# Kernel optimization log

Hardware: AMD Instinct MI355X
Metric: run time of the kernel (lower is better)

## Reference

```python
import jax, jax.numpy as jnp
import numpy as np

B, T, I, H = 64, 512, 1024, 1024


def setup_inputs() -> dict:
    key = jax.random.key(0)
    ks = jax.random.split(key, 6)
    s_ih = 1.0 / np.sqrt(I)
    s_hh = 1.0 / np.sqrt(H)
    x = jax.random.normal(ks[0], (B, T, I), dtype=jnp.float32)
    w_ih = jax.random.uniform(ks[1], (4 * H, I), minval=-s_ih, maxval=s_ih, dtype=jnp.float32)
    b_ih = jax.random.uniform(ks[2], (4 * H,), minval=-s_ih, maxval=s_ih, dtype=jnp.float32)
    w_hh = jax.random.uniform(ks[3], (4 * H, H), minval=-s_hh, maxval=s_hh, dtype=jnp.float32)
    b_hh = jax.random.uniform(ks[4], (4 * H,), minval=-s_hh, maxval=s_hh, dtype=jnp.float32)
    # forget_bias = logit(u), u ~ Uniform(1/H, 1-1/H), as in init_hidden
    u = jax.random.uniform(ks[5], (H,), minval=1.0 / H, maxval=1.0 - 1.0 / H, dtype=jnp.float32)
    forget_bias = jnp.log(u / (1.0 - u))
    h0 = jnp.zeros((B, H), dtype=jnp.float32)
    c0 = jnp.zeros((B, H), dtype=jnp.float32)
    return {"x": x, "w_ih": w_ih, "b_ih": b_ih, "w_hh": w_hh, "b_hh": b_hh,
            "forget_bias": forget_bias, "h0": h0, "c0": c0}


def reference(x, w_ih, b_ih, w_hh, b_hh, forget_bias, h0, c0):
    Hd = forget_bias.shape[0]
    # Precompute input projection for all timesteps: [T, B, 4H]
    xW = jnp.einsum('bti,gi->tbg', x, w_ih) + b_ih

    def step(carry, xw_t):
        h, c = carry
        lin = xw_t + h @ w_hh.T + b_hh  # [B, 4H]
        r, f, u, o = jnp.split(lin, 4, axis=1)
        r = jax.nn.sigmoid(r - forget_bias)
        f = jax.nn.sigmoid(f + forget_bias)
        u = jnp.tanh(u)
        o = jax.nn.sigmoid(o)
        g = r * (1.0 - (1.0 - f) ** 2) + (1.0 - r) * f ** 2  # UR gate
        c = g * c + (1.0 - g) * u
        h = o * jnp.tanh(c)
        return (h, c), h

    (h_t, c_t), out = jax.lax.scan(step, (h0, c0), xW)
    out = jnp.swapaxes(out, 0, 1)  # [B, T, H]
    return out, h_t[None], c_t[None]  # h/c with num_layers=1 leading dim
```

## Files before the change

kernel.cpp:

```cpp
#include <hip/hip_runtime.h>
#include <stdint.h>
#include <stddef.h>

typedef __attribute__((ext_vector_type(8))) short short8;
typedef __attribute__((ext_vector_type(4))) float f32x4;
typedef __attribute__((ext_vector_type(2))) float f32x2;

#define MFMA16(A, B, C) __builtin_amdgcn_mfma_f32_16x16x32_bf16((A), (B), (C), 0, 0, 0)

static const size_t OFF_XB   = 0;
static const size_t OFF_WIH  = 67108864;
static const size_t OFF_WHH  = 75497472;
static const size_t OFF_BIAS = 83886080;
static const size_t OFF_H0   = 83902464;
static const size_t OFF_H1   = 84033536;
static const size_t OFF_FLG  = 84164608;
static const size_t OFF_XW   = 84426752;
static const size_t XW_F32_BYTES = 536870912;

__device__ __forceinline__ unsigned short f2bf(float f) {
    union { float f; uint32_t u; } v; v.f = f;
    uint32_t u = v.u;
    u += 0x7FFFu + ((u >> 16) & 1u);
    return (unsigned short)(u >> 16);
}
__device__ __forceinline__ float bf2f(unsigned short b) {
    union { uint32_t u; float f; } v; v.u = ((uint32_t)b) << 16;
    return v.f;
}

__device__ __forceinline__ float fast_sigmoid(float x) {
    return 1.f / (1.f + __expf(-x));
}
__device__ __forceinline__ float fast_tanh(float x) {
    return 1.f - 2.f / (__expf(2.f * x) + 1.f);
}

__global__ __launch_bounds__(256) void cast4_kernel(const float* __restrict__ s,
                                                    unsigned short* __restrict__ d, int n4) {
    int i = blockIdx.x * 256 + threadIdx.x;
    if (i >= n4) return;
    float4 f = ((const float4*)s)[i];
    ushort4 o;
    o.x = f2bf(f.x); o.y = f2bf(f.y); o.z = f2bf(f.z); o.w = f2bf(f.w);
    ((ushort4*)d)[i] = o;
}

__global__ __launch_bounds__(256) void init_misc(const float* __restrict__ b_ih,
                                                 const float* __restrict__ b_hh,
                                                 float* __restrict__ bias,
                                                 const float* __restrict__ h0,
                                                 unsigned short* __restrict__ h_ini,
                                                 unsigned int* __restrict__ flags) {
    int i = blockIdx.x * 256 + threadIdx.x;
    if (i < 512) flags[i] = 0u;
    if (i < 4096) bias[i] = b_ih[i] + b_hh[i];
    if (i < 65536) h_ini[i] = f2bf(h0[i]);
}

template <bool XWF32>
__global__ __launch_bounds__(256) void xw_gemm(const unsigned short* __restrict__ xb,
                                               const unsigned short* __restrict__ wb,
                                               const float* __restrict__ bias,
                                               void* __restrict__ xw) {
    __shared__ __align__(16) unsigned short As[128 * 32];
    __shared__ __align__(16) unsigned short Bs[128 * 32];
    const int bm = blockIdx.x, bn = blockIdx.y;
    const int tid = threadIdx.x;
    const int wave = tid >> 6, lane = tid & 63;
    const int wm = (wave >> 1) * 64, wn = (wave & 1) * 64;
    const int lr = lane & 15, lk = (lane >> 4) * 8;

    const int c0 = tid, c1 = tid + 256;
    const int r0 = c0 >> 2, k0c = (c0 & 3) * 8;
    const int r1 = c1 >> 2, k1c = (c1 & 3) * 8;
    const int mA0 = bm * 128 + r0, mA1 = bm * 128 + r1;
    const unsigned short* pa0 = xb + (size_t)(((mA0 & 63) << 9) + (mA0 >> 6)) * 1024 + k0c;
    const unsigned short* pa1 = xb + (size_t)(((mA1 & 63) << 9) + (mA1 >> 6)) * 1024 + k1c;
    const unsigned short* pb0 = wb + (size_t)(bn * 128 + r0) * 1024 + k0c;
    const unsigned short* pb1 = wb + (size_t)(bn * 128 + r1) * 1024 + k1c;
    unsigned short* sa0 = As + r0 * 32 + k0c;
    unsigned short* sa1 = As + r1 * 32 + k1c;
    unsigned short* sb0 = Bs + r0 * 32 + k0c;
    unsigned short* sb1 = Bs + r1 * 32 + k1c;

    f32x4 acc[4][4] = {};

    for (int kk = 0; kk < 32; ++kk) {
        const int ko = kk * 32;
        uint4 av0 = *(const uint4*)(pa0 + ko);
        uint4 av1 = *(const uint4*)(pa1 + ko);
        uint4 bv0 = *(const uint4*)(pb0 + ko);
        uint4 bv1 = *(const uint4*)(pb1 + ko);
        __syncthreads();
        *(uint4*)sa0 = av0;
        *(uint4*)sa1 = av1;
        *(uint4*)sb0 = bv0;
        *(uint4*)sb1 = bv1;
        __syncthreads();
        short8 af[4], bfr[4];
#pragma unroll
        for (int mi = 0; mi < 4; ++mi)
            af[mi] = *(const short8*)(As + (wm + mi * 16 + lr) * 32 + lk);
#pragma unroll
        for (int ni = 0; ni < 4; ++ni)
            bfr[ni] = *(const short8*)(Bs + (wn + ni * 16 + lr) * 32 + lk);
#pragma unroll
        for (int mi = 0; mi < 4; ++mi)
#pragma unroll
            for (int ni = 0; ni < 4; ++ni)
                acc[mi][ni] = MFMA16(af[mi], bfr[ni], acc[mi][ni]);
    }

    const int rbase = (lane >> 4) * 4;
#pragma unroll
    for (int ni = 0; ni < 4; ++ni) {
        const int gc = bn * 128 + wn + ni * 16 + lr;
        const float bv = bias[gc];
#pragma unroll
        for (int mi = 0; mi < 4; ++mi) {
            const int gr = bm * 128 + wm + mi * 16 + rbase;
#pragma unroll
            for (int r = 0; r < 4; ++r) {
                float v = acc[mi][ni][r] + bv;
                if (XWF32) ((float*)xw)[(size_t)(gr + r) * 4096 + gc] = v;
                else ((unsigned short*)xw)[(size_t)(gr + r) * 4096 + gc] = f2bf(v);
            }
        }
    }
}

template <bool XWF32>
__global__ __launch_bounds__(512, 2) void lstm_persistent(
        unsigned short* hb0, unsigned short* hb1,
        const void* __restrict__ xw,
        const unsigned short* __restrict__ whh,
        const float* __restrict__ fb,
        const float* __restrict__ c0,
        float* __restrict__ out,
        float* __restrict__ hcout,
        unsigned int* ctr) {
    __shared__ __align__(16) float part[8 * 64 * 64];

    const int tid = threadIdx.x;
    const int wave = tid >> 6, lane = tid & 63;
    const int bk = blockIdx.x, ch0 = bk * 16;
    const int kq = wave;
    const int lr = lane & 15, g = lane >> 4;

    short8 Wf[4][4];
#pragma unroll
    for (int ni = 0; ni < 4; ++ni)
#pragma unroll
        for (int ks = 0; ks < 4; ++ks) {
            const unsigned short* p = whh + (size_t)(ni * 1024 + ch0 + lr) * 1024
                                          + kq * 128 + ks * 32 + g * 8;
            asm volatile("global_load_dwordx4 %0, %1, off"
                         : "=&v"(Wf[ni][ks]) : "v"(p));
        }
    asm volatile("s_waitcnt vmcnt(0)" ::: "memory");
    __builtin_amdgcn_sched_barrier(0);

    const int b  = tid >> 3;
    const int j0 = 2 * (tid & 7);
    const int ch = ch0 + j0;
    const float fb0 = fb[ch], fb1 = fb[ch + 1];
    float c0r = c0[b * 1024 + ch], c1r = c0[b * 1024 + ch + 1];

    int wsl[4];
#pragma unroll
    for (int oi = 0; oi < 4; ++oi)
        wsl[oi] = kq * 4096 + lr * 64 + (((oi * 4 + g) ^ (lr & 7)) * 4);
    int rsl[4];
#pragma unroll
    for (int g4 = 0; g4 < 4; ++g4)
        rsl[g4] = b * 64 + (((g4 * 4 + (j0 >> 2)) ^ (b & 7)) * 4) + (j0 & 3);

    const float* xwf = (const float*)xw + (size_t)b * 4096 + ch;
    const unsigned short* xwb = (const unsigned short*)xw + (size_t)b * 4096 + ch;
    float* orun = out + (size_t)b * 524288 + ch;
    unsigned int* my_sig  = &ctr[(bk >> 3) * 32];
    unsigned int* my_poll = &ctr[kq * 32];

    float xwv0[4], xwv1[4];
#pragma unroll
    for (int g4 = 0; g4 < 4; ++g4) {
        if constexpr (XWF32) {
            const f32x2 v = *(const f32x2*)(xwf + g4 * 1024);
            xwv0[g4] = v.x; xwv1[g4] = v.y;
        } else {
            const uint32_t u = *(const uint32_t*)(xwb + g4 * 1024);
            xwv0[g4] = bf2f((unsigned short)u);
            xwv1[g4] = bf2f((unsigned short)(u >> 16));
        }
    }

    float h0v = 0.f, h1v = 0.f;

    for (int t = 0; t < 512; ++t) {
        const unsigned short* hp = (t & 1) ? hb1 : hb0;
        unsigned short* hn       = (t & 1) ? hb0 : hb1;

        if (t > 0) {
            const unsigned tgt = (unsigned)t * 8u;
            while (__hip_atomic_load(my_poll, __ATOMIC_RELAXED,
                                     __HIP_MEMORY_SCOPE_AGENT) < tgt) {}
        }
        __builtin_amdgcn_sched_barrier(0);

        short8 af[4][4];
        {
            const unsigned short* hbase = hp + (size_t)lr * 1024 + kq * 128 + g * 8;
#pragma unroll
            for (int bi = 0; bi < 4; ++bi) {
                const unsigned short* p = hbase + (size_t)bi * 16 * 1024;
                asm volatile(
                    "global_load_dwordx4 %0, %4, off sc1\n\t"
                    "global_load_dwordx4 %1, %4, off offset:64 sc1\n\t"
                    "global_load_dwordx4 %2, %4, off offset:128 sc1\n\t"
                    "global_load_dwordx4 %3, %4, off offset:192 sc1"
                    : "=&v"(af[bi][0]), "=&v"(af[bi][1]),
                      "=&v"(af[bi][2]), "=&v"(af[bi][3])
                    : "v"(p));
            }
        }
        asm volatile("s_waitcnt vmcnt(0)" ::: "memory");
        __builtin_amdgcn_sched_barrier(0);

        f32x4 acc[4][4] = {};
#pragma unroll
        for (int ks = 0; ks < 4; ++ks)
#pragma unroll
            for (int oi = 0; oi < 4; ++oi)
#pragma unroll
                for (int bi = 0; bi < 4; ++bi)
                    acc[oi][bi] = MFMA16(Wf[oi][ks], af[bi][ks], acc[oi][bi]);

#pragma unroll
        for (int oi = 0; oi < 4; ++oi)
#pragma unroll
            for (int bi = 0; bi < 4; ++bi)
                *(f32x4*)&part[wsl[oi] + bi * 1024] = acc[oi][bi];
        __syncthreads();

        float l0[4], l1[4];
#pragma unroll
        for (int g4 = 0; g4 < 4; ++g4) {
            float s0 = xwv0[g4], s1 = xwv1[g4];
#pragma unroll
            for (int k8 = 0; k8 < 8; ++k8) {
                const float2 v = *(const float2*)&part[k8 * 4096 + rsl[g4]];
                s0 += v.x; s1 += v.y;
            }
            l0[g4] = s0; l1[g4] = s1;
        }
        const float rg0 = fast_sigmoid(l0[0] - fb0);
        const float fg0 = fast_sigmoid(l0[1] + fb0);
        const float ug0 = fast_tanh(l0[2]);
        const float og0 = fast_sigmoid(l0[3]);
        const float rg1 = fast_sigmoid(l1[0] - fb1);
        const float fg1 = fast_sigmoid(l1[1] + fb1);
        const float ug1 = fast_tanh(l1[2]);
        const float og1 = fast_sigmoid(l1[3]);
        const float of0 = 1.f - fg0, of1 = 1.f - fg1;
        const float gg0 = rg0 * (1.f - of0 * of0) + (1.f - rg0) * (fg0 * fg0);
        const float gg1 = rg1 * (1.f - of1 * of1) + (1.f - rg1) * (fg1 * fg1);
        c0r = gg0 * c0r + (1.f - gg0) * ug0;
        c1r = gg1 * c1r + (1.f - gg1) * ug1;
        h0v = og0 * fast_tanh(c0r);
        h1v = og1 * fast_tanh(c1r);

        const unsigned hw = ((unsigned)f2bf(h1v) << 16) | (unsigned)f2bf(h0v);
        __hip_atomic_store((unsigned int*)&hn[b * 1024 + ch], hw,
                           __ATOMIC_RELAXED, __HIP_MEMORY_SCOPE_AGENT);

        __syncthreads();
        if (tid == 0)
            __hip_atomic_fetch_add(my_sig, 1u, __ATOMIC_RELAXED,
                                   __HIP_MEMORY_SCOPE_AGENT);
        __builtin_amdgcn_sched_barrier(0);

        *(f32x2*)orun = (f32x2){h0v, h1v};
        orun += 1024;
        {
            const int tp = (t < 511) ? t + 1 : 511;
#pragma unroll
            for (int g4 = 0; g4 < 4; ++g4) {
                if constexpr (XWF32) {
                    const f32x2 v = *(const f32x2*)(xwf + (size_t)tp * 262144 + g4 * 1024);
                    xwv0[g4] = v.x; xwv1[g4] = v.y;
                } else {
                    const uint32_t u = *(const uint32_t*)(xwb + (size_t)tp * 262144 + g4 * 1024);
                    xwv0[g4] = bf2f((unsigned short)u);
                    xwv1[g4] = bf2f((unsigned short)(u >> 16));
                }
            }
        }
        asm volatile("s_waitcnt vmcnt(0)" ::: "memory");
        __builtin_amdgcn_sched_barrier(0);
    }

    *(f32x2*)&hcout[b * 1024 + ch] = (f32x2){h0v, h1v};
    *(f32x2*)&hcout[65536 + b * 1024 + ch] = (f32x2){c0r, c1r};
}

extern "C" void kernel_launch(void* const* d_in, const int* in_sizes, int n_in,
                              void* d_out, int out_size, void* d_ws, size_t ws_size,
                              hipStream_t stream) {
    const float* x   = (const float*)d_in[0];
    const float* wih = (const float*)d_in[1];
    const float* bih = (const float*)d_in[2];
    const float* whh = (const float*)d_in[3];
    const float* bhh = (const float*)d_in[4];
    const float* fb  = (const float*)d_in[5];
    const float* h0  = (const float*)d_in[6];
    const float* c0  = (const float*)d_in[7];

    char* ws = (char*)d_ws;
    float* out = (float*)d_out;
    float* hc  = out + 33554432;

    unsigned short* xb   = (unsigned short*)(ws + OFF_XB);
    unsigned short* wihb = (unsigned short*)(ws + OFF_WIH);
    unsigned short* whhb = (unsigned short*)(ws + OFF_WHH);
    float* bias          = (float*)(ws + OFF_BIAS);
    unsigned short* hb0  = (unsigned short*)(ws + OFF_H0);
    unsigned short* hb1  = (unsigned short*)(ws + OFF_H1);
    unsigned int* flags  = (unsigned int*)(ws + OFF_FLG);
    void* xw             = (void*)(ws + OFF_XW);

    const bool f32path = ws_size >= OFF_XW + XW_F32_BYTES;

    cast4_kernel<<<32768, 256, 0, stream>>>(x, xb, 8388608);
    cast4_kernel<<<4096, 256, 0, stream>>>(wih, wihb, 1048576);
    cast4_kernel<<<4096, 256, 0, stream>>>(whh, whhb, 1048576);
    init_misc<<<256, 256, 0, stream>>>(bih, bhh, bias, h0, hb0, flags);

    dim3 g(256, 32);
    if (f32path) xw_gemm<true><<<g, 256, 0, stream>>>(xb, wihb, bias, xw);
    else         xw_gemm<false><<<g, 256, 0, stream>>>(xb, wihb, bias, xw);

    const float* fbp = fb;
    const float* c0p = c0;
    void* xwp = xw;
    const unsigned short* whhp = whhb;
    unsigned int* ctr = flags;
    void* kargs[] = { &hb0, &hb1, &xwp, &whhp, &fbp, &c0p, &out, &hc, &ctr };
    if (f32path)
        hipLaunchCooperativeKernel((void*)lstm_persistent<true>, dim3(64), dim3(512),
                                   kargs, 0, stream);
    else
        hipLaunchCooperativeKernel((void*)lstm_persistent<false>, dim3(64), dim3(512),
                                   kargs, 0, stream);
}
```

Measured before the change: 4.169 ms.

## Split batch into two halves with separate flags to overlap recurrent phases

Each timestep is now processed as two 32-row batch halves, each with its own arrival counter. The B-half loads are issued before the A-half's reduction and gate math, and the A-half's h is published with its own signal before the B-half MFMAs run. The aim is to let other blocks start the next step on half A while half B is still computing, hiding inter-block sync latency. The cost is twice as many barriers, polls and atomics per step, narrower scalar stores, and reliance on the counter array being large enough for a second bank at offset 256.

```diff
diff --git a/kernel.cpp b/kernel.cpp
--- a/kernel.cpp
+++ b/kernel.cpp
@@ -140,7 +140,7 @@
         float* __restrict__ out,
         float* __restrict__ hcout,
         unsigned int* ctr) {
-    __shared__ __align__(16) float part[8 * 64 * 64];
+    __shared__ __align__(16) float part[8 * 32 * 64];
 
     const int tid = threadIdx.x;
     const int wave = tid >> 6, lane = tid & 63;
@@ -161,147 +161,209 @@
     asm volatile("s_waitcnt vmcnt(0)" ::: "memory");
     __builtin_amdgcn_sched_barrier(0);
 
-    const int b  = tid >> 3;
-    const int j0 = 2 * (tid & 7);
-    const int ch = ch0 + j0;
-    const float fb0 = fb[ch], fb1 = fb[ch + 1];
-    float c0r = c0[b * 1024 + ch], c1r = c0[b * 1024 + ch + 1];
+    const int jj = tid & 15;
+    const int bb = tid >> 4;
+    const int ch = ch0 + jj;
+    const float fbv = fb[ch];
+    float cA = c0[bb * 1024 + ch];
+    float cB = c0[(32 + bb) * 1024 + ch];
 
     int wsl[4];
 #pragma unroll
     for (int oi = 0; oi < 4; ++oi)
-        wsl[oi] = kq * 4096 + lr * 64 + (((oi * 4 + g) ^ (lr & 7)) * 4);
+        wsl[oi] = kq * 2048 + lr * 64 + ((((oi * 4 + g) ^ (lr & 7))) << 2);
     int rsl[4];
 #pragma unroll
     for (int g4 = 0; g4 < 4; ++g4)
-        rsl[g4] = b * 64 + (((g4 * 4 + (j0 >> 2)) ^ (b & 7)) * 4) + (j0 & 3);
-
-    const float* xwf = (const float*)xw + (size_t)b * 4096 + ch;
-    const unsigned short* xwb = (const unsigned short*)xw + (size_t)b * 4096 + ch;
-    float* orun = out + (size_t)b * 524288 + ch;
-    unsigned int* my_sig  = &ctr[(bk >> 3) * 32];
-    unsigned int* my_poll = &ctr[kq * 32];
-
-    float xwv0[4], xwv1[4];
+        rsl[g4] = bb * 64 + ((((g4 * 4 + (jj >> 2)) ^ (bb & 7))) << 2) + (jj & 3);
+
+    const float* xw32 = (const float*)xw;
+    const unsigned short* xw16 = (const unsigned short*)xw;
+    const size_t xbA = (size_t)bb * 4096 + ch;
+    const size_t xbB = (size_t)(32 + bb) * 4096 + ch;
+    float* orA = out + (size_t)bb * 524288 + ch;
+    float* orB = out + (size_t)(32 + bb) * 524288 + ch;
+    unsigned int* sigA = &ctr[(bk >> 3) * 32];
+    unsigned int* sigB = &ctr[256 + (bk >> 3) * 32];
+    unsigned int* polA = &ctr[kq * 32];
+    unsigned int* polB = &ctr[256 + kq * 32];
+
+    float xwA[4], xwB[4];
 #pragma unroll
     for (int g4 = 0; g4 < 4; ++g4) {
         if constexpr (XWF32) {
-            const f32x2 v = *(const f32x2*)(xwf + g4 * 1024);
-            xwv0[g4] = v.x; xwv1[g4] = v.y;
+            xwA[g4] = xw32[xbA + g4 * 1024];
+            xwB[g4] = xw32[xbB + g4 * 1024];
         } else {
-            const uint32_t u = *(const uint32_t*)(xwb + g4 * 1024);
-            xwv0[g4] = bf2f((unsigned short)u);
-            xwv1[g4] = bf2f((unsigned short)(u >> 16));
+            xwA[g4] = bf2f(xw16[xbA + g4 * 1024]);
+            xwB[g4] = bf2f(xw16[xbB + g4 * 1024]);
         }
     }
 
-    float h0v = 0.f, h1v = 0.f;
+    float hA = 0.f, hB = 0.f;
 
     for (int t = 0; t < 512; ++t) {
         const unsigned short* hp = (t & 1) ? hb1 : hb0;
         unsigned short* hn       = (t & 1) ? hb0 : hb1;
+        const unsigned short* hbase = hp + (size_t)lr * 1024 + kq * 128 + g * 8;
 
         if (t > 0) {
             const unsigned tgt = (unsigned)t * 8u;
-            while (__hip_atomic_load(my_poll, __ATOMIC_RELAXED,
+            while (__hip_atomic_load(polA, __ATOMIC_RELAXED,
                                      __HIP_MEMORY_SCOPE_AGENT) < tgt) {}
         }
         __builtin_amdgcn_sched_barrier(0);
 
-        short8 af[4][4];
+        short8 afA[2][4];
+#pragma unroll
+        for (int bi = 0; bi < 2; ++bi) {
+            const unsigned short* p = hbase + (size_t)bi * 16 * 1024;
+            asm volatile(
+                "global_load_dwordx4 %0, %4, off sc1\n\t"
+                "global_load_dwordx4 %1, %4, off offset:64 sc1\n\t"
+                "global_load_dwordx4 %2, %4, off offset:128 sc1\n\t"
+                "global_load_dwordx4 %3, %4, off offset:192 sc1"
+                : "=&v"(afA[bi][0]), "=&v"(afA[bi][1]),
+                  "=&v"(afA[bi][2]), "=&v"(afA[bi][3])
+                : "v"(p));
+        }
+        asm volatile("s_waitcnt vmcnt(0)" ::: "memory");
+        __builtin_amdgcn_sched_barrier(0);
+
         {
-            const unsigned short* hbase = hp + (size_t)lr * 1024 + kq * 128 + g * 8;
-#pragma unroll
-            for (int bi = 0; bi < 4; ++bi) {
-                const unsigned short* p = hbase + (size_t)bi * 16 * 1024;
-                asm volatile(
-                    "global_load_dwordx4 %0, %4, off sc1\n\t"
-                    "global_load_dwordx4 %1, %4, off offset:64 sc1\n\t"
-                    "global_load_dwordx4 %2, %4, off offset:128 sc1\n\t"
-                    "global_load_dwordx4 %3, %4, off offset:192 sc1"
-                    : "=&v"(af[bi][0]), "=&v"(af[bi][1]),
-                      "=&v"(af[bi][2]), "=&v"(af[bi][3])
-                    : "v"(p));
+            f32x4 acc[4][2] = {};
+#pragma unroll
+            for (int ks = 0; ks < 4; ++ks)
+#pragma unroll
+                for (int oi = 0; oi < 4; ++oi)
+#pragma unroll
+                    for (int bi = 0; bi < 2; ++bi)
+                        acc[oi][bi] = MFMA16(Wf[oi][ks], afA[bi][ks], acc[oi][bi]);
+#pragma unroll
+            for (int oi = 0; oi < 4; ++oi)
+#pragma unroll
+                for (int bi = 0; bi < 2; ++bi)
+                    *(f32x4*)&part[wsl[oi] + bi * 1024] = acc[oi][bi];
+        }
+        __syncthreads();
+
+        if (t > 0) {
+            const unsigned tgt = (unsigned)t * 8u;
+            while (__hip_atomic_load(polB, __ATOMIC_RELAXED,
+                                     __HIP_MEMORY_SCOPE_AGENT) < tgt) {}
+        }
+        __builtin_amdgcn_sched_barrier(0);
+        short8 afB[2][4];
+#pragma unroll
+        for (int bi = 0; bi < 2; ++bi) {
+            const unsigned short* p = hbase + (size_t)(32 + bi * 16) * 1024;
+            asm volatile(
+                "global_load_dwordx4 %0, %4, off sc1\n\t"
+                "global_load_dwordx4 %1, %4, off offset:64 sc1\n\t"
+                "global_load_dwordx4 %2, %4, off offset:128 sc1\n\t"
+                "global_load_dwordx4 %3, %4, off offset:192 sc1"
+                : "=&v"(afB[bi][0]), "=&v"(afB[bi][1]),
+                  "=&v"(afB[bi][2]), "=&v"(afB[bi][3])
+                : "v"(p));
+        }
+        __builtin_amdgcn_sched_barrier(0);
+
+        {
+            float l[4];
+#pragma unroll
+            for (int g4 = 0; g4 < 4; ++g4) {
+                float s = xwA[g4];
+#pragma unroll
+                for (int k8 = 0; k8 < 8; ++k8)
+                    s += part[k8 * 2048 + rsl[g4]];
+                l[g4] = s;
             }
+            const float rg = fast_sigmoid(l[0] - fbv);
+            const float fg = fast_sigmoid(l[1] + fbv);
+            const float ug = fast_tanh(l[2]);
+            const float og = fast_sigmoid(l[3]);
+            const float of = 1.f - fg;
+            const float gg = rg * (1.f - of * of) + (1.f - rg) * (fg * fg);
+            cA = gg * cA + (1.f - gg) * ug;
+            hA = og * fast_tanh(cA);
+            const unsigned hw = (unsigned)f2bf(hA);
+            asm volatile("global_store_short %0, %1, off sc1"
+                         :: "v"(hn + bb * 1024 + ch), "v"(hw) : "memory");
         }
         asm volatile("s_waitcnt vmcnt(0)" ::: "memory");
-        __builtin_amdgcn_sched_barrier(0);
-
-        f32x4 acc[4][4] = {};
-#pragma unroll
-        for (int ks = 0; ks < 4; ++ks)
+        __syncthreads();
+        if (tid == 0)
+            __hip_atomic_fetch_add(sigA, 1u, __ATOMIC_RELAXED, __HIP_MEMORY_SCOPE_AGENT);
+        __builtin_amdgcn_sched_barrier(0);
+
+        {
+            f32x4 acc[4][2] = {};
+#pragma unroll
+            for (int ks = 0; ks < 4; ++ks)
+#pragma unroll
+                for (int oi = 0; oi < 4; ++oi)
+#pragma unroll
+                    for (int bi = 0; bi < 2; ++bi)
+                        acc[oi][bi] = MFMA16(Wf[oi][ks], afB[bi][ks], acc[oi][bi]);
 #pragma unroll
             for (int oi = 0; oi < 4; ++oi)
 #pragma unroll
-                for (int bi = 0; bi < 4; ++bi)
-                    acc[oi][bi] = MFMA16(Wf[oi][ks], af[bi][ks], acc[oi][bi]);
-
-#pragma unroll
-        for (int oi = 0; oi < 4; ++oi)
-#pragma unroll
-            for (int bi = 0; bi < 4; ++bi)
-                *(f32x4*)&part[wsl[oi] + bi * 1024] = acc[oi][bi];
-        __syncthreads();
-
-        float l0[4], l1[4];
-#pragma unroll
-        for (int g4 = 0; g4 < 4; ++g4) {
-            float s0 = xwv0[g4], s1 = xwv1[g4];
-#pragma unroll
-            for (int k8 = 0; k8 < 8; ++k8) {
-                const float2 v = *(const float2*)&part[k8 * 4096 + rsl[g4]];
-                s0 += v.x; s1 += v.y;
+                for (int bi = 0; bi < 2; ++bi)
+                    *(f32x4*)&part[wsl[oi] + bi * 1024] = acc[oi][bi];
+        }
+        __syncthreads();
+
+        {
+            float l[4];
+#pragma unroll
+            for (int g4 = 0; g4 < 4; ++g4) {
+                float s = xwB[g4];
+#pragma unroll
+                for (int k8 = 0; k8 < 8; ++k8)
+                    s += part[k8 * 2048 + rsl[g4]];
+                l[g4] = s;
             }
-            l0[g4] = s0; l1[g4] = s1;
-        }
-        const float rg0 = fast_sigmoid(l0[0] - fb0);
-        const float fg0 = fast_sigmoid(l0[1] + fb0);
-        const float ug0 = fast_tanh(l0[2]);
-        const float og0 = fast_sigmoid(l0[3]);
-        const float rg1 = fast_sigmoid(l1[0] - fb1);
-        const float fg1 = fast_sigmoid(l1[1] + fb1);
-        const float ug1 = fast_tanh(l1[2]);
-        const float og1 = fast_sigmoid(l1[3]);
-        const float of0 = 1.f - fg0, of1 = 1.f - fg1;
-        const float gg0 = rg0 * (1.f - of0 * of0) + (1.f - rg0) * (fg0 * fg0);
-        const float gg1 = rg1 * (1.f - of1 * of1) + (1.f - rg1) * (fg1 * fg1);
-        c0r = gg0 * c0r + (1.f - gg0) * ug0;
-        c1r = gg1 * c1r + (1.f - gg1) * ug1;
-        h0v = og0 * fast_tanh(c0r);
-        h1v = og1 * fast_tanh(c1r);
-
-        const unsigned hw = ((unsigned)f2bf(h1v) << 16) | (unsigned)f2bf(h0v);
-        __hip_atomic_store((unsigned int*)&hn[b * 1024 + ch], hw,
-                           __ATOMIC_RELAXED, __HIP_MEMORY_SCOPE_AGENT);
-
+            const float rg = fast_sigmoid(l[0] - fbv);
+            const float fg = fast_sigmoid(l[1] + fbv);
+            const float ug = fast_tanh(l[2]);
+            const float og = fast_sigmoid(l[3]);
+            const float of = 1.f - fg;
+            const float gg = rg * (1.f - of * of) + (1.f - rg) * (fg * fg);
+            cB = gg * cB + (1.f - gg) * ug;
+            hB = og * fast_tanh(cB);
+            const unsigned hw = (unsigned)f2bf(hB);
+            asm volatile("global_store_short %0, %1, off sc1"
+                         :: "v"(hn + (32 + bb) * 1024 + ch), "v"(hw) : "memory");
+        }
+        asm volatile("s_waitcnt vmcnt(0)" ::: "memory");
         __syncthreads();
         if (tid == 0)
-            __hip_atomic_fetch_add(my_sig, 1u, __ATOMIC_RELAXED,
-                                   __HIP_MEMORY_SCOPE_AGENT);
-        __builtin_amdgcn_sched_barrier(0);
-
-        *(f32x2*)orun = (f32x2){h0v, h1v};
-        orun += 1024;
+            __hip_atomic_fetch_add(sigB, 1u, __ATOMIC_RELAXED, __HIP_MEMORY_SCOPE_AGENT);
+        __builtin_amdgcn_sched_barrier(0);
+
+        *orA = hA; orA += 1024;
+        *orB = hB; orB += 1024;
         {
             const int tp = (t < 511) ? t + 1 : 511;
+            const size_t tb = (size_t)tp * 262144;
 #pragma unroll
             for (int g4 = 0; g4 < 4; ++g4) {
                 if constexpr (XWF32) {
-                    const f32x2 v = *(const f32x2*)(xwf + (size_t)tp * 262144 + g4 * 1024);
-                    xwv0[g4] = v.x; xwv1[g4] = v.y;
+                    xwA[g4] = xw32[tb + xbA + g4 * 1024];
+                    xwB[g4] = xw32[tb + xbB + g4 * 1024];
                 } else {
-                    const uint32_t u = *(const uint32_t*)(xwb + (size_t)tp * 262144 + g4 * 1024);
-                    xwv0[g4] = bf2f((unsigned short)u);
-                    xwv1[g4] = bf2f((unsigned short)(u >> 16));
+                    xwA[g4] = bf2f(xw16[tb + xbA + g4 * 1024]);
+                    xwB[g4] = bf2f(xw16[tb + xbB + g4 * 1024]);
                 }
             }
         }
-        asm volatile("s_waitcnt vmcnt(0)" ::: "memory");
         __builtin_amdgcn_sched_barrier(0);
     }
 
-    *(f32x2*)&hcout[b * 1024 + ch] = (f32x2){h0v, h1v};
-    *(f32x2*)&hcout[65536 + b * 1024 + ch] = (f32x2){c0r, c1r};
+    hcout[bb * 1024 + ch] = hA;
+    hcout[65536 + bb * 1024 + ch] = cA;
+    hcout[(32 + bb) * 1024 + ch] = hB;
+    hcout[65536 + (32 + bb) * 1024 + ch] = cB;
 }
 
 extern "C" void kernel_launch(void* const* d_in, const int* in_sizes, int n_in,
```

Result: slower. 4.626 ms (+11.0%).

## Fuse input-projection GEMM into persistent LSTM kernel with producer/consumer flags

Applied to the files above, without the earlier changes.

Merges the xW GEMM into the cooperative recurrence kernel: 64 blocks run the LSTM recurrence while 192 extra blocks compute xW tiles in time order and signal per-row-block progress counters that the recurrent blocks poll before loading each timestep. The x fp32-to-bf16 cast is folded into the GEMM tile load, which removes the separate cast pass and the extra bf16 copy of x. The goal is to overlap the large projection GEMM with the serial recurrence. In exchange, the GEMM blocks compete with the recurrent blocks for memory bandwidth and CUs. The recurrence may also stall on progress flags if the GEMM falls behind. The flag region now shares the init flag array at offset 256.

```diff
diff --git a/kernel.cpp b/kernel.cpp
--- a/kernel.cpp
+++ b/kernel.cpp
@@ -8,7 +8,6 @@
 
 #define MFMA16(A, B, C) __builtin_amdgcn_mfma_f32_16x16x32_bf16((A), (B), (C), 0, 0, 0)
 
-static const size_t OFF_XB   = 0;
 static const size_t OFF_WIH  = 67108864;
 static const size_t OFF_WHH  = 75497472;
 static const size_t OFF_BIAS = 83886080;
@@ -59,94 +58,103 @@
 }
 
 template <bool XWF32>
-__global__ __launch_bounds__(256) void xw_gemm(const unsigned short* __restrict__ xb,
-                                               const unsigned short* __restrict__ wb,
-                                               const float* __restrict__ bias,
-                                               void* __restrict__ xw) {
-    __shared__ __align__(16) unsigned short As[128 * 32];
-    __shared__ __align__(16) unsigned short Bs[128 * 32];
-    const int bm = blockIdx.x, bn = blockIdx.y;
-    const int tid = threadIdx.x;
-    const int wave = tid >> 6, lane = tid & 63;
-    const int wm = (wave >> 1) * 64, wn = (wave & 1) * 64;
-    const int lr = lane & 15, lk = (lane >> 4) * 8;
-
-    const int c0 = tid, c1 = tid + 256;
-    const int r0 = c0 >> 2, k0c = (c0 & 3) * 8;
-    const int r1 = c1 >> 2, k1c = (c1 & 3) * 8;
-    const int mA0 = bm * 128 + r0, mA1 = bm * 128 + r1;
-    const unsigned short* pa0 = xb + (size_t)(((mA0 & 63) << 9) + (mA0 >> 6)) * 1024 + k0c;
-    const unsigned short* pa1 = xb + (size_t)(((mA1 & 63) << 9) + (mA1 >> 6)) * 1024 + k1c;
-    const unsigned short* pb0 = wb + (size_t)(bn * 128 + r0) * 1024 + k0c;
-    const unsigned short* pb1 = wb + (size_t)(bn * 128 + r1) * 1024 + k1c;
-    unsigned short* sa0 = As + r0 * 32 + k0c;
-    unsigned short* sa1 = As + r1 * 32 + k1c;
-    unsigned short* sb0 = Bs + r0 * 32 + k0c;
-    unsigned short* sb1 = Bs + r1 * 32 + k1c;
-
-    f32x4 acc[4][4] = {};
-
-    for (int kk = 0; kk < 32; ++kk) {
-        const int ko = kk * 32;
-        uint4 av0 = *(const uint4*)(pa0 + ko);
-        uint4 av1 = *(const uint4*)(pa1 + ko);
-        uint4 bv0 = *(const uint4*)(pb0 + ko);
-        uint4 bv1 = *(const uint4*)(pb1 + ko);
-        __syncthreads();
-        *(uint4*)sa0 = av0;
-        *(uint4*)sa1 = av1;
-        *(uint4*)sb0 = bv0;
-        *(uint4*)sb1 = bv1;
-        __syncthreads();
-        short8 af[4], bfr[4];
-#pragma unroll
-        for (int mi = 0; mi < 4; ++mi)
-            af[mi] = *(const short8*)(As + (wm + mi * 16 + lr) * 32 + lk);
-#pragma unroll
-        for (int ni = 0; ni < 4; ++ni)
-            bfr[ni] = *(const short8*)(Bs + (wn + ni * 16 + lr) * 32 + lk);
-#pragma unroll
-        for (int mi = 0; mi < 4; ++mi)
-#pragma unroll
-            for (int ni = 0; ni < 4; ++ni)
-                acc[mi][ni] = MFMA16(af[mi], bfr[ni], acc[mi][ni]);
-    }
-
-    const int rbase = (lane >> 4) * 4;
-#pragma unroll
-    for (int ni = 0; ni < 4; ++ni) {
-        const int gc = bn * 128 + wn + ni * 16 + lr;
-        const float bv = bias[gc];
-#pragma unroll
-        for (int mi = 0; mi < 4; ++mi) {
-            const int gr = bm * 128 + wm + mi * 16 + rbase;
-#pragma unroll
-            for (int r = 0; r < 4; ++r) {
-                float v = acc[mi][ni][r] + bv;
-                if (XWF32) ((float*)xw)[(size_t)(gr + r) * 4096 + gc] = v;
-                else ((unsigned short*)xw)[(size_t)(gr + r) * 4096 + gc] = f2bf(v);
-            }
-        }
-    }
-}
-
-template <bool XWF32>
-__global__ __launch_bounds__(512, 2) void lstm_persistent(
+__global__ __launch_bounds__(512, 2) void fused_kernel(
         unsigned short* hb0, unsigned short* hb1,
-        const void* __restrict__ xw,
+        void* xw,
         const unsigned short* __restrict__ whh,
+        const unsigned short* __restrict__ wih,
+        const float* __restrict__ x,
+        const float* __restrict__ bias,
         const float* __restrict__ fb,
         const float* __restrict__ c0,
         float* __restrict__ out,
         float* __restrict__ hcout,
-        unsigned int* ctr) {
-    __shared__ __align__(16) float part[8 * 64 * 64];
-
+        unsigned int* flags) {
+    __shared__ __align__(16) char smem[131072];
     const int tid = threadIdx.x;
     const int wave = tid >> 6, lane = tid & 63;
+    unsigned int* xwprog = flags + 256;
+
+    if (blockIdx.x >= 64) {
+        unsigned short* As = (unsigned short*)smem;
+        unsigned short* Bs = (unsigned short*)(smem + 8192);
+        const int g = blockIdx.x - 64;
+        const int wm = (wave & 3) * 32, wn = (wave >> 2) * 64;
+        const int lr = lane & 15, lk = (lane >> 4) * 8;
+        const int r0 = tid >> 2, k0c = (tid & 3) * 8;
+        const int rbase = (lane >> 4) * 4;
+
+        for (int tau = g; tau < 8192; tau += 192) {
+            const int bm = tau >> 5, bn = tau & 31;
+            const int m = bm * 128 + r0;
+            const float* pax = x + (size_t)((m & 63) * 512 + (m >> 6)) * 1024 + k0c;
+            const unsigned short* pbw = wih + (size_t)(bn * 128 + r0) * 1024 + k0c;
+            unsigned short* sa = As + r0 * 32 + k0c;
+            unsigned short* sb = Bs + r0 * 32 + k0c;
+
+            f32x4 acc[2][4] = {};
+            for (int kk = 0; kk < 32; ++kk) {
+                const int ko = kk * 32;
+                float4 a0 = *(const float4*)(pax + ko);
+                float4 a1 = *(const float4*)(pax + ko + 4);
+                uint4 bv = *(const uint4*)(pbw + ko);
+                __syncthreads();
+                ushort4 ca, cb;
+                ca.x = f2bf(a0.x); ca.y = f2bf(a0.y); ca.z = f2bf(a0.z); ca.w = f2bf(a0.w);
+                cb.x = f2bf(a1.x); cb.y = f2bf(a1.y); cb.z = f2bf(a1.z); cb.w = f2bf(a1.w);
+                *(ushort4*)sa = ca;
+                *(ushort4*)(sa + 4) = cb;
+                *(uint4*)sb = bv;
+                __syncthreads();
+                short8 af0 = *(const short8*)(As + (wm + lr) * 32 + lk);
+                short8 af1 = *(const short8*)(As + (wm + 16 + lr) * 32 + lk);
+                short8 bf4[4];
+#pragma unroll
+                for (int ni = 0; ni < 4; ++ni)
+                    bf4[ni] = *(const short8*)(Bs + (wn + ni * 16 + lr) * 32 + lk);
+#pragma unroll
+                for (int ni = 0; ni < 4; ++ni) {
+                    acc[0][ni] = MFMA16(af0, bf4[ni], acc[0][ni]);
+                    acc[1][ni] = MFMA16(af1, bf4[ni], acc[1][ni]);
+                }
+            }
+#pragma unroll
+            for (int ni = 0; ni < 4; ++ni) {
+                const int gc = bn * 128 + wn + ni * 16 + lr;
+                const float bvs = bias[gc];
+#pragma unroll
+                for (int mi = 0; mi < 2; ++mi) {
+                    const int gr = bm * 128 + wm + mi * 16 + rbase;
+#pragma unroll
+                    for (int r = 0; r < 4; ++r) {
+                        const float v = acc[mi][ni][r] + bvs;
+                        if constexpr (XWF32) {
+                            float* p = (float*)xw + (size_t)(gr + r) * 4096 + gc;
+                            asm volatile("global_store_dword %0, %1, off sc1"
+                                         :: "v"(p), "v"(v) : "memory");
+                        } else {
+                            unsigned short* p = (unsigned short*)xw + (size_t)(gr + r) * 4096 + gc;
+                            const unsigned int hv = f2bf(v);
+                            asm volatile("global_store_short %0, %1, off sc1"
+                                         :: "v"(p), "v"(hv) : "memory");
+                        }
+                    }
+                }
+            }
+            asm volatile("s_waitcnt vmcnt(0)" ::: "memory");
+            __syncthreads();
+            if (tid == 0)
+                __hip_atomic_fetch_add(&xwprog[bm], 1u, __ATOMIC_RELAXED,
+                                       __HIP_MEMORY_SCOPE_AGENT);
+        }
+        return;
+    }
+
+    float* part = (float*)smem;
     const int bk = blockIdx.x, ch0 = bk * 16;
     const int kq = wave;
     const int lr = lane & 15, g = lane >> 4;
+    unsigned int* ctr = flags;
 
     short8 Wf[4][4];
 #pragma unroll
@@ -182,18 +190,32 @@
     unsigned int* my_sig  = &ctr[(bk >> 3) * 32];
     unsigned int* my_poll = &ctr[kq * 32];
 
-    float xwv0[4], xwv1[4];
-#pragma unroll
-    for (int g4 = 0; g4 < 4; ++g4) {
-        if constexpr (XWF32) {
-            const f32x2 v = *(const f32x2*)(xwf + g4 * 1024);
-            xwv0[g4] = v.x; xwv1[g4] = v.y;
-        } else {
-            const uint32_t u = *(const uint32_t*)(xwb + g4 * 1024);
-            xwv0[g4] = bf2f((unsigned short)u);
-            xwv1[g4] = bf2f((unsigned short)(u >> 16));
-        }
+    {
+        const unsigned int* pr0 = &xwprog[0];
+        while (__hip_atomic_load(pr0, __ATOMIC_RELAXED, __HIP_MEMORY_SCOPE_AGENT) < 32u) {}
     }
+    __builtin_amdgcn_sched_barrier(0);
+    f32x2 xf[4];
+    uint32_t xu[4];
+    if constexpr (XWF32) {
+        asm volatile(
+            "global_load_dwordx2 %0, %4, off sc1\n\t"
+            "global_load_dwordx2 %1, %5, off sc1\n\t"
+            "global_load_dwordx2 %2, %6, off sc1\n\t"
+            "global_load_dwordx2 %3, %7, off sc1"
+            : "=&v"(xf[0]), "=&v"(xf[1]), "=&v"(xf[2]), "=&v"(xf[3])
+            : "v"(xwf), "v"(xwf + 1024), "v"(xwf + 2048), "v"(xwf + 3072));
+    } else {
+        asm volatile(
+            "global_load_dword %0, %4, off sc1\n\t"
+            "global_load_dword %1, %5, off sc1\n\t"
+            "global_load_dword %2, %6, off sc1\n\t"
+            "global_load_dword %3, %7, off sc1"
+            : "=&v"(xu[0]), "=&v"(xu[1]), "=&v"(xu[2]), "=&v"(xu[3])
+            : "v"(xwb), "v"(xwb + 1024), "v"(xwb + 2048), "v"(xwb + 3072));
+    }
+    asm volatile("s_waitcnt vmcnt(0)" ::: "memory");
+    __builtin_amdgcn_sched_barrier(0);
 
     float h0v = 0.f, h1v = 0.f;
 
@@ -246,7 +268,10 @@
         float l0[4], l1[4];
 #pragma unroll
         for (int g4 = 0; g4 < 4; ++g4) {
-            float s0 = xwv0[g4], s1 = xwv1[g4];
+            float s0, s1;
+            if constexpr (XWF32) { s0 = xf[g4].x; s1 = xf[g4].y; }
+            else { s0 = bf2f((unsigned short)xu[g4]);
+                   s1 = bf2f((unsigned short)(xu[g4] >> 16)); }
 #pragma unroll
             for (int k8 = 0; k8 < 8; ++k8) {
                 const float2 v = *(const float2*)&part[k8 * 4096 + rsl[g4]];
@@ -284,16 +309,29 @@
         orun += 1024;
         {
             const int tp = (t < 511) ? t + 1 : 511;
-#pragma unroll
-            for (int g4 = 0; g4 < 4; ++g4) {
-                if constexpr (XWF32) {
-                    const f32x2 v = *(const f32x2*)(xwf + (size_t)tp * 262144 + g4 * 1024);
-                    xwv0[g4] = v.x; xwv1[g4] = v.y;
-                } else {
-                    const uint32_t u = *(const uint32_t*)(xwb + (size_t)tp * 262144 + g4 * 1024);
-                    xwv0[g4] = bf2f((unsigned short)u);
-                    xwv1[g4] = bf2f((unsigned short)(u >> 16));
-                }
+            if (!(tp & 1)) {
+                const unsigned int* pr = &xwprog[tp >> 1];
+                while (__hip_atomic_load(pr, __ATOMIC_RELAXED,
+                                         __HIP_MEMORY_SCOPE_AGENT) < 32u) {}
+            }
+            if constexpr (XWF32) {
+                const float* p0 = xwf + (size_t)tp * 262144;
+                asm volatile(
+                    "global_load_dwordx2 %0, %4, off sc1\n\t"
+                    "global_load_dwordx2 %1, %5, off sc1\n\t"
+                    "global_load_dwordx2 %2, %6, off sc1\n\t"
+                    "global_load_dwordx2 %3, %7, off sc1"
+                    : "=&v"(xf[0]), "=&v"(xf[1]), "=&v"(xf[2]), "=&v"(xf[3])
+                    : "v"(p0), "v"(p0 + 1024), "v"(p0 + 2048), "v"(p0 + 3072));
+            } else {
+                const unsigned short* p0 = xwb + (size_t)tp * 262144;
+                asm volatile(
+                    "global_load_dword %0, %4, off sc1\n\t"
+                    "global_load_dword %1, %5, off sc1\n\t"
+                    "global_load_dword %2, %6, off sc1\n\t"
+                    "global_load_dword %3, %7, off sc1"
+                    : "=&v"(xu[0]), "=&v"(xu[1]), "=&v"(xu[2]), "=&v"(xu[3])
+                    : "v"(p0), "v"(p0 + 1024), "v"(p0 + 2048), "v"(p0 + 3072));
             }
         }
         asm volatile("s_waitcnt vmcnt(0)" ::: "memory");
@@ -320,7 +358,6 @@
     float* out = (float*)d_out;
     float* hc  = out + 33554432;
 
-    unsigned short* xb   = (unsigned short*)(ws + OFF_XB);
     unsigned short* wihb = (unsigned short*)(ws + OFF_WIH);
     unsigned short* whhb = (unsigned short*)(ws + OFF_WHH);
     float* bias          = (float*)(ws + OFF_BIAS);
@@ -331,25 +368,23 @@
 
     const bool f32path = ws_size >= OFF_XW + XW_F32_BYTES;
 
-    cast4_kernel<<<32768, 256, 0, stream>>>(x, xb, 8388608);
     cast4_kernel<<<4096, 256, 0, stream>>>(wih, wihb, 1048576);
     cast4_kernel<<<4096, 256, 0, stream>>>(whh, whhb, 1048576);
     init_misc<<<256, 256, 0, stream>>>(bih, bhh, bias, h0, hb0, flags);
 
-    dim3 g(256, 32);
-    if (f32path) xw_gemm<true><<<g, 256, 0, stream>>>(xb, wihb, bias, xw);
-    else         xw_gemm<false><<<g, 256, 0, stream>>>(xb, wihb, bias, xw);
-
+    const float* xp = x;
     const float* fbp = fb;
     const float* c0p = c0;
     void* xwp = xw;
     const unsigned short* whhp = whhb;
-    unsigned int* ctr = flags;
-    void* kargs[] = { &hb0, &hb1, &xwp, &whhp, &fbp, &c0p, &out, &hc, &ctr };
+    const unsigned short* wihp = wihb;
+    const float* biasp = bias;
+    void* kargs[] = { &hb0, &hb1, &xwp, &whhp, &wihp, &xp, &biasp, &fbp, &c0p,
+                      &out, &hc, &flags };
     if (f32path)
-        hipLaunchCooperativeKernel((void*)lstm_persistent<true>, dim3(64), dim3(512),
+        hipLaunchCooperativeKernel((void*)fused_kernel<true>, dim3(256), dim3(512),
                                    kargs, 0, stream);
     else
-        hipLaunchCooperativeKernel((void*)lstm_persistent<false>, dim3(64), dim3(512),
+        hipLaunchCooperativeKernel((void*)fused_kernel<false>, dim3(256), dim3(512),
                                    kargs, 0, stream);
 }
```

Result: faster. 3.690 ms, median of 2 (-11.5%).
